# Performance work log

Hardware: AMD Instinct MI355X
Metric: run time of the kernel (lower is better)

## Reference

```python
import jax, jax.numpy as jnp
import numpy as np
import math

EPS = 1e-5

def _ln(x, g, b):
    mu = jnp.mean(x, axis=-1, keepdims=True)
    var = jnp.mean((x - mu) ** 2, axis=-1, keepdims=True)
    return (x - mu) * jax.lax.rsqrt(var + EPS) * g + b

def _phasor(x, phases, wv, bv, lno_g, lno_b, wo, bo):
    # x: [B,L,D]; phases buffer: [max_seq_len,D]
    B, L, D = x.shape
    ph = phases[:L][None]            # [1,L,D]
    c, s = jnp.cos(ph), jnp.sin(ph)
    v = x @ wv + bv                  # [B,L,D]
    mem_r = jnp.cumsum(v * c, axis=1)
    mem_i = jnp.cumsum(v * s, axis=1)
    retrieved = (mem_r * c + mem_i * s) / math.sqrt(D)
    return x + _ln(retrieved, lno_g, lno_b) @ wo + bo

def setup_inputs() -> dict:
    key = jax.random.key(0)
    ks = jax.random.split(key, 10)
    V, D, S, B, L = 32000, 1024, 2048, 4, 2048
    sc = 1.0 / math.sqrt(D)
    return {
        "tokens": jax.random.randint(ks[0], (B, L), 0, V, dtype=jnp.int32),
        "embed": jax.random.normal(ks[1], (V, D), jnp.float32) * sc,
        "ln1_g": jnp.ones((D,), jnp.float32), "ln1_b": jnp.zeros((D,), jnp.float32),
        "ph1": jax.random.normal(ks[2], (S, D), jnp.float32) * math.pi,
        "wv1": jax.random.normal(ks[3], (D, D), jnp.float32) * sc,
        "bv1": jnp.zeros((D,), jnp.float32),
        "lno1_g": jnp.ones((D,), jnp.float32), "lno1_b": jnp.zeros((D,), jnp.float32),
        "wo1": jax.random.normal(ks[4], (D, D), jnp.float32) * sc,
        "bo1": jnp.zeros((D,), jnp.float32),
        "ln2_g": jnp.ones((D,), jnp.float32), "ln2_b": jnp.zeros((D,), jnp.float32),
        "ph2": jax.random.normal(ks[5], (S, D), jnp.float32) * math.pi,
        "wv2": jax.random.normal(ks[6], (D, D), jnp.float32) * sc,
        "bv2": jnp.zeros((D,), jnp.float32),
        "lno2_g": jnp.ones((D,), jnp.float32), "lno2_b": jnp.zeros((D,), jnp.float32),
        "wo2": jax.random.normal(ks[7], (D, D), jnp.float32) * sc,
        "bo2": jnp.zeros((D,), jnp.float32),
        "ln3_g": jnp.ones((D,), jnp.float32), "ln3_b": jnp.zeros((D,), jnp.float32),
        "w_head": jax.random.normal(ks[8], (D, V), jnp.float32) * sc,
        "b_head": jnp.zeros((V,), jnp.float32),
    }

def reference(tokens, embed, ln1_g, ln1_b, ph1, wv1, bv1, lno1_g, lno1_b, wo1, bo1,
              ln2_g, ln2_b, ph2, wv2, bv2, lno2_g, lno2_b, wo2, bo2,
              ln3_g, ln3_b, w_head, b_head):
    h = embed[tokens]                                  # [B,L,D]
    h = h + _phasor(_ln(h, ln1_g, ln1_b), ph1, wv1, bv1, lno1_g, lno1_b, wo1, bo1)
    h = h + _phasor(_ln(h, ln2_g, ln2_b), ph2, wv2, bv2, lno2_g, lno2_b, wo2, bo2)
    return _ln(h, ln3_g, ln3_b) @ w_head + b_head      # [B,L,V]
```

## Files before the change

### kernel.cpp

```cpp
#include <hip/hip_runtime.h>
#include <hip/hip_bf16.h>
#include <math.h>

typedef __hip_bfloat16 bf16;
typedef __attribute__((ext_vector_type(8))) short bf16x8;
typedef __attribute__((ext_vector_type(4))) float f32x4;

#define GPTR(p) ((__attribute__((address_space(1))) void*)(void*)(p))
#define LPTR(p) ((__attribute__((address_space(3))) void*)(void*)(p))

static constexpr int kB = 4, kL = 2048, kD = 1024, kV = 32000;
static constexpr int kM = kB * kL;
static constexpr int kNC = 16, kCH = kL / kNC;

__global__ void k_sincos(const float* __restrict__ ph, float* __restrict__ c,
                         float* __restrict__ s, int n) {
  int i = blockIdx.x * 256 + threadIdx.x;
  if (i < n) {
    float sv, cv;
    sincosf(ph[i], &sv, &cv);
    c[i] = cv;
    s[i] = sv;
  }
}

__global__ void k_tcvt64(const float* __restrict__ in, bf16* __restrict__ out,
                         int R, int C) {
  __shared__ bf16 tile[64][66];
  int c0 = blockIdx.x * 64, r0 = blockIdx.y * 64;
  int tid = threadIdx.x;
  int cq = tid & 15;
  int rr = tid >> 4;
#pragma unroll
  for (int i = 0; i < 4; i++) {
    int r = rr + i * 16;
    float4 v = *(const float4*)(in + (size_t)(r0 + r) * C + c0 + cq * 4);
    tile[r][cq * 4 + 0] = __float2bfloat16(v.x);
    tile[r][cq * 4 + 1] = __float2bfloat16(v.y);
    tile[r][cq * 4 + 2] = __float2bfloat16(v.z);
    tile[r][cq * 4 + 3] = __float2bfloat16(v.w);
  }
  __syncthreads();
  int rb = tid & 7;
  int cc = tid >> 3;
#pragma unroll
  for (int i = 0; i < 2; i++) {
    int c = cc + i * 32;
    bf16x8 p;
#pragma unroll
    for (int j = 0; j < 8; j++) p[j] = *(const short*)&tile[rb * 8 + j][c];
    *(bf16x8*)(out + (size_t)(c0 + c) * R + r0 + rb * 8) = p;
  }
}

__global__ void k_embln(const int* __restrict__ tok, const float* __restrict__ emb,
                        const float* __restrict__ g, const float* __restrict__ b,
                        float* __restrict__ h, bf16* __restrict__ ob,
                        float* __restrict__ of) {
  int row = blockIdx.x;
  int tid = threadIdx.x;
  int t = tok[row];
  float4 v = ((const float4*)(emb + (size_t)t * kD))[tid];
  ((float4*)(h + (size_t)row * kD))[tid] = v;
  float sum = v.x + v.y + v.z + v.w;
  float sq = fmaf(v.x, v.x, fmaf(v.y, v.y, fmaf(v.z, v.z, v.w * v.w)));
#pragma unroll
  for (int o = 32; o > 0; o >>= 1) {
    sum += __shfl_down(sum, o);
    sq += __shfl_down(sq, o);
  }
  __shared__ float ss[4], sk[4];
  int w = tid >> 6;
  if ((tid & 63) == 0) { ss[w] = sum; sk[w] = sq; }
  __syncthreads();
  float ts = ss[0] + ss[1] + ss[2] + ss[3];
  float tq = sk[0] + sk[1] + sk[2] + sk[3];
  float mu = ts * (1.0f / kD);
  float var = tq * (1.0f / kD) - mu * mu;
  float rstd = rsqrtf(var + 1e-5f);
  float4 gg = ((const float4*)g)[tid];
  float4 bb = ((const float4*)b)[tid];
  float4 o;
  o.x = fmaf((v.x - mu) * rstd, gg.x, bb.x);
  o.y = fmaf((v.y - mu) * rstd, gg.y, bb.y);
  o.z = fmaf((v.z - mu) * rstd, gg.z, bb.z);
  o.w = fmaf((v.w - mu) * rstd, gg.w, bb.w);
  union { ushort4 u; bf16 hh[4]; } pk;
  pk.hh[0] = __float2bfloat16(o.x);
  pk.hh[1] = __float2bfloat16(o.y);
  pk.hh[2] = __float2bfloat16(o.z);
  pk.hh[3] = __float2bfloat16(o.w);
  *(ushort4*)(ob + (size_t)row * kD + tid * 4) = pk.u;
  ((float4*)(of + (size_t)row * kD))[tid] = o;
}

template <bool WF32>
__global__ void k_ln(const float* __restrict__ in, const float* __restrict__ g,
                     const float* __restrict__ b, bf16* __restrict__ ob,
                     float* __restrict__ of) {
  int row = blockIdx.x;
  int tid = threadIdx.x;
  const float4* x4 = (const float4*)(in + (size_t)row * kD);
  float4 v = x4[tid];
  float sum = v.x + v.y + v.z + v.w;
  float sq = fmaf(v.x, v.x, fmaf(v.y, v.y, fmaf(v.z, v.z, v.w * v.w)));
#pragma unroll
  for (int o = 32; o > 0; o >>= 1) {
    sum += __shfl_down(sum, o);
    sq += __shfl_down(sq, o);
  }
  __shared__ float ss[4], sk[4];
  int w = tid >> 6;
  if ((tid & 63) == 0) { ss[w] = sum; sk[w] = sq; }
  __syncthreads();
  float ts = ss[0] + ss[1] + ss[2] + ss[3];
  float tq = sk[0] + sk[1] + sk[2] + sk[3];
  float mu = ts * (1.0f / kD);
  float var = tq * (1.0f / kD) - mu * mu;
  float rstd = rsqrtf(var + 1e-5f);
  float4 gg = ((const float4*)g)[tid];
  float4 bb = ((const float4*)b)[tid];
  float4 o;
  o.x = fmaf((v.x - mu) * rstd, gg.x, bb.x);
  o.y = fmaf((v.y - mu) * rstd, gg.y, bb.y);
  o.z = fmaf((v.z - mu) * rstd, gg.z, bb.z);
  o.w = fmaf((v.w - mu) * rstd, gg.w, bb.w);
  union { ushort4 u; bf16 h[4]; } pk;
  pk.h[0] = __float2bfloat16(o.x);
  pk.h[1] = __float2bfloat16(o.y);
  pk.h[2] = __float2bfloat16(o.z);
  pk.h[3] = __float2bfloat16(o.w);
  *(ushort4*)(ob + (size_t)row * kD + tid * 4) = pk.u;
  if constexpr (WF32) {
    ((float4*)(of + (size_t)row * kD))[tid] = o;
  }
}

__global__ void k_scan_part(const float* __restrict__ v, const float* __restrict__ c,
                            const float* __restrict__ s, float* __restrict__ pr,
                            float* __restrict__ pi) {
  int tid = blockIdx.x * 256 + threadIdx.x;
  int d = tid & (kD - 1);
  int ch = (tid >> 10) & (kNC - 1);
  int b = tid >> 14;
  const float* vp = v + ((size_t)b * kL + ch * kCH) * kD + d;
  const float* cp = c + (size_t)(ch * kCH) * kD + d;
  const float* sp = s + (size_t)(ch * kCH) * kD + d;
  float ar = 0.f, ai = 0.f;
  for (int i = 0; i < kCH; i++) {
    float vv = vp[i * kD];
    ar = fmaf(vv, cp[i * kD], ar);
    ai = fmaf(vv, sp[i * kD], ai);
  }
  pr[tid] = ar;
  pi[tid] = ai;
}

__global__ void k_scan_apply(float* __restrict__ v, const float* __restrict__ c,
                             const float* __restrict__ s, const float* __restrict__ pr,
                             const float* __restrict__ pi) {
  int tid = blockIdx.x * 256 + threadIdx.x;
  int d = tid & (kD - 1);
  int ch = (tid >> 10) & (kNC - 1);
  int b = tid >> 14;
  float ar = 0.f, ai = 0.f;
  int pbase = (b << 14) + d;
  for (int cc = 0; cc < ch; cc++) {
    ar += pr[pbase + cc * kD];
    ai += pi[pbase + cc * kD];
  }
  float* vp = v + ((size_t)b * kL + ch * kCH) * kD + d;
  const float* cp = c + (size_t)(ch * kCH) * kD + d;
  const float* sp = s + (size_t)(ch * kCH) * kD + d;
  for (int i = 0; i < kCH; i++) {
    float vv = vp[i * kD];
    float cv = cp[i * kD], sv = sp[i * kD];
    ar = fmaf(vv, cv, ar);
    ai = fmaf(vv, sv, ai);
    vp[i * kD] = (ar * cv + ai * sv) * 0.03125f;
  }
}

template <int MODE>
__global__ __launch_bounds__(256) void k_gemm_bt(
    const bf16* __restrict__ A, const bf16* __restrict__ BT,
    const float* __restrict__ bias, const float* __restrict__ xres,
    const float* __restrict__ hres, float* __restrict__ Cout,
    int Md, int Nd, int Kd) {
  __shared__ __align__(16) bf16 As[128 * 32];
  __shared__ __align__(16) bf16 Bs[128 * 32];
  int nwg = gridDim.x * gridDim.y;
  int wg = blockIdx.y * gridDim.x + blockIdx.x;
  int per = nwg >> 3;
  int sw = (wg & 7) * per + (wg >> 3);
  int bm = sw % gridDim.x;
  int bn = sw / gridDim.x;
  int m0 = bm * 128, n0 = bn * 128;
  int tid = threadIdx.x;
  int wid = tid >> 6, lane = tid & 63;
  int wr = wid >> 1, wc = wid & 1;

  f32x4 acc[4][4];
#pragma unroll
  for (int i = 0; i < 4; i++)
#pragma unroll
    for (int j = 0; j < 4; j++) acc[i][j] = (f32x4){0.f, 0.f, 0.f, 0.f};

  const bf16* Abase = A + (size_t)m0 * Kd;
  const bf16* Bbase = BT + (size_t)n0 * Kd;
  int lr = lane >> 2;
  int lk = (lane & 3) * 8;
  int frow = lane & 15;
  int fk = (lane >> 4) * 8;

  for (int k0 = 0; k0 < Kd; k0 += 32) {
#pragma unroll
    for (int c = 0; c < 2; c++) {
      int ch = wid + c * 4;
      __builtin_amdgcn_global_load_lds(GPTR(Abase + (size_t)(ch * 16 + lr) * Kd + k0 + lk),
                                       LPTR(As + ch * 512), 16, 0, 0);
      __builtin_amdgcn_global_load_lds(GPTR(Bbase + (size_t)(ch * 16 + lr) * Kd + k0 + lk),
                                       LPTR(Bs + ch * 512), 16, 0, 0);
    }
    asm volatile("s_waitcnt vmcnt(0)" ::: "memory");
    __syncthreads();
    bf16x8 af[4], bfr[4];
#pragma unroll
    for (int i = 0; i < 4; i++) {
      af[i] = *(const bf16x8*)(As + (wr * 64 + i * 16 + frow) * 32 + fk);
      bfr[i] = *(const bf16x8*)(Bs + (wc * 64 + i * 16 + frow) * 32 + fk);
    }
#pragma unroll
    for (int i = 0; i < 4; i++)
#pragma unroll
      for (int j = 0; j < 4; j++)
        acc[i][j] = __builtin_amdgcn_mfma_f32_16x16x32_bf16(af[i], bfr[j], acc[i][j], 0, 0, 0);
    __syncthreads();
  }

  int cr = (lane >> 4) * 4;
  int ccl = lane & 15;
#pragma unroll
  for (int i = 0; i < 4; i++) {
#pragma unroll
    for (int j = 0; j < 4; j++) {
      int col = n0 + wc * 64 + j * 16 + ccl;
      float bv = bias[col];
#pragma unroll
      for (int r = 0; r < 4; r++) {
        int row = m0 + wr * 64 + i * 16 + cr + r;
        size_t idx = (size_t)row * Nd + col;
        float val = acc[i][j][r] + bv;
        if (MODE == 1) val += hres[idx] + xres[idx];
        Cout[idx] = val;
      }
    }
  }
}

__global__ __launch_bounds__(512, 2) void k_gemm256p8(
    const bf16* __restrict__ A, const bf16* __restrict__ BT,
    const float* __restrict__ bias, float* __restrict__ Cout,
    int Md, int Nd, int Kd) {
  __shared__ __align__(16) bf16 As[2][16384];
  __shared__ __align__(16) bf16 Bs[2][16384];

  int gx = gridDim.x;
  int wg = blockIdx.y * gx + blockIdx.x;
  int mch = gx >> 3;
  int xcd = wg & 7;
  int r = wg >> 3;
  int bm = xcd * mch + (r % mch);
  int bn = r / mch;
  int m0 = bm * 256, n0 = bn * 256;

  int tid = threadIdx.x;
  int wid = tid >> 6, lane = tid & 63;
  int wr = wid >> 2, wc = wid & 3;

  size_t KdS = (size_t)Kd;
  int srow = tid >> 3;
  int sk = (((tid & 7) ^ (srow & 7)) << 3);
  const bf16* aSrc = A + (size_t)(m0 + srow) * KdS + sk;
  const bf16* bSrc = BT + (size_t)(n0 + srow) * KdS + sk;
  int ldst = wid * 512;

#define STAGE_A(buf, h, t)                                                              \
  do {                                                                                  \
    __builtin_amdgcn_global_load_lds(GPTR(aSrc + (size_t)((h) * 128) * KdS + (t) * 64), \
                                     LPTR(&As[buf][(h) * 8192 + ldst]), 16, 0, 0);      \
    __builtin_amdgcn_global_load_lds(                                                   \
        GPTR(aSrc + (size_t)((h) * 128 + 64) * KdS + (t) * 64),                         \
        LPTR(&As[buf][(h) * 8192 + 4096 + ldst]), 16, 0, 0);                            \
  } while (0)
#define STAGE_B(buf, h, t)                                                              \
  do {                                                                                  \
    __builtin_amdgcn_global_load_lds(GPTR(bSrc + (size_t)((h) * 128) * KdS + (t) * 64), \
                                     LPTR(&Bs[buf][(h) * 8192 + ldst]), 16, 0, 0);      \
    __builtin_amdgcn_global_load_lds(                                                   \
        GPTR(bSrc + (size_t)((h) * 128 + 64) * KdS + (t) * 64),                         \
        LPTR(&Bs[buf][(h) * 8192 + 4096 + ldst]), 16, 0, 0);                            \
  } while (0)

  int frow = lane & 15;
  int khi = lane >> 4;
  int rx = frow & 7;
  int lk0 = ((khi) ^ rx) << 3;
  int lk1 = ((4 + khi) ^ rx) << 3;
  int wr16 = wr * 16;
  int wc64 = wc * 64;

  f32x4 acc[8][4];
#pragma unroll
  for (int m = 0; m < 8; m++)
#pragma unroll
    for (int n = 0; n < 4; n++) acc[m][n] = (f32x4){0.f, 0.f, 0.f, 0.f};

  const int NT = Kd >> 6;

  STAGE_A(0, 0, 0);
  STAGE_B(0, 0, 0);
  STAGE_B(0, 1, 0);
  STAGE_A(0, 1, 0);
  STAGE_A(1, 0, 1);
  STAGE_B(1, 0, 1);
  STAGE_B(1, 1, 1);
  asm volatile("s_waitcnt vmcnt(6)" ::: "memory");
  __builtin_amdgcn_s_barrier();
  __builtin_amdgcn_sched_barrier(0);

  for (int t = 0; t < NT; ++t) {
    int c = t & 1, o = c ^ 1;
    const bf16* Ac = As[c];
    const bf16* Bc = Bs[c];
    bf16x8 a[4][2], b[2][2], b2[2][2];

#pragma unroll
    for (int m = 0; m < 4; m++) {
      int ro = (m * 32 + wr16 + frow) * 64;
      a[m][0] = *(const bf16x8*)(Ac + ro + lk0);
      a[m][1] = *(const bf16x8*)(Ac + ro + lk1);
    }
#pragma unroll
    for (int n = 0; n < 2; n++) {
      int ro = (wc64 + n * 16 + frow) * 64;
      b[n][0] = *(const bf16x8*)(Bc + ro + lk0);
      b[n][1] = *(const bf16x8*)(Bc + ro + lk1);
    }
    if (t + 1 < NT) STAGE_A(o, 1, t + 1);
    __builtin_amdgcn_s_barrier();
    asm volatile("s_waitcnt lgkmcnt(0)" ::: "memory");
    __builtin_amdgcn_sched_barrier(0);
    __builtin_amdgcn_s_setprio(1);
#pragma unroll
    for (int m = 0; m < 4; m++)
#pragma unroll
      for (int n = 0; n < 2; n++) {
        acc[m][n] = __builtin_amdgcn_mfma_f32_16x16x32_bf16(a[m][0], b[n][0], acc[m][n], 0, 0, 0);
        acc[m][n] = __builtin_amdgcn_mfma_f32_16x16x32_bf16(a[m][1], b[n][1], acc[m][n], 0, 0, 0);
      }
    __builtin_amdgcn_s_setprio(0);
    __builtin_amdgcn_s_barrier();
    __builtin_amdgcn_sched_barrier(0);

#pragma unroll
    for (int n = 0; n < 2; n++) {
      int ro = (wc64 + (n + 2) * 16 + frow) * 64;
      b2[n][0] = *(const bf16x8*)(Bc + ro + lk0);
      b2[n][1] = *(const bf16x8*)(Bc + ro + lk1);
    }
    if (t + 2 < NT) STAGE_A(c, 0, t + 2);
    __builtin_amdgcn_s_barrier();
    asm volatile("s_waitcnt lgkmcnt(0)" ::: "memory");
    __builtin_amdgcn_sched_barrier(0);
    __builtin_amdgcn_s_setprio(1);
#pragma unroll
    for (int m = 0; m < 4; m++)
#pragma unroll
      for (int n = 0; n < 2; n++) {
        acc[m][n + 2] = __builtin_amdgcn_mfma_f32_16x16x32_bf16(a[m][0], b2[n][0], acc[m][n + 2], 0, 0, 0);
        acc[m][n + 2] = __builtin_amdgcn_mfma_f32_16x16x32_bf16(a[m][1], b2[n][1], acc[m][n + 2], 0, 0, 0);
      }
    __builtin_amdgcn_s_setprio(0);
    __builtin_amdgcn_s_barrier();
    __builtin_amdgcn_sched_barrier(0);

#pragma unroll
    for (int m = 0; m < 4; m++) {
      int ro = ((m + 4) * 32 + wr16 + frow) * 64;
      a[m][0] = *(const bf16x8*)(Ac + ro + lk0);
      a[m][1] = *(const bf16x8*)(Ac + ro + lk1);
    }
    if (t + 2 < NT) STAGE_B(c, 0, t + 2);
    __builtin_amdgcn_s_barrier();
    asm volatile("s_waitcnt lgkmcnt(0)" ::: "memory");
    __builtin_amdgcn_sched_barrier(0);
    __builtin_amdgcn_s_setprio(1);
#pragma unroll
    for (int m = 0; m < 4; m++)
#pragma unroll
      for (int n = 0; n < 2; n++) {
        acc[m + 4][n] = __builtin_amdgcn_mfma_f32_16x16x32_bf16(a[m][0], b[n][0], acc[m + 4][n], 0, 0, 0);
        acc[m + 4][n] = __builtin_amdgcn_mfma_f32_16x16x32_bf16(a[m][1], b[n][1], acc[m + 4][n], 0, 0, 0);
      }
    __builtin_amdgcn_s_setprio(0);
    __builtin_amdgcn_s_barrier();
    __builtin_amdgcn_sched_barrier(0);

    if (t + 2 < NT) STAGE_B(c, 1, t + 2);
    __builtin_amdgcn_s_barrier();
    __builtin_amdgcn_sched_barrier(0);
    __builtin_amdgcn_s_setprio(1);
#pragma unroll
    for (int m = 0; m < 4; m++)
#pragma unroll
      for (int n = 0; n < 2; n++) {
        acc[m + 4][n + 2] = __builtin_amdgcn_mfma_f32_16x16x32_bf16(a[m][0], b2[n][0], acc[m + 4][n + 2], 0, 0, 0);
        acc[m + 4][n + 2] = __builtin_amdgcn_mfma_f32_16x16x32_bf16(a[m][1], b2[n][1], acc[m + 4][n + 2], 0, 0, 0);
      }
    __builtin_amdgcn_s_setprio(0);
    if (t < NT - 2) {
      asm volatile("s_waitcnt vmcnt(6)" ::: "memory");
    } else if (t == NT - 2) {
      asm volatile("s_waitcnt vmcnt(0)" ::: "memory");
    }
    __builtin_amdgcn_s_barrier();
    __builtin_amdgcn_sched_barrier(0);
  }
#undef STAGE_A
#undef STAGE_B

  float* eplds = (float*)&As[0][0] + wid * 1088;
  int q = lane & 15;
  int g = lane >> 4;
  float bv[4];
#pragma unroll
  for (int n = 0; n < 4; n++) bv[n] = bias[n0 + wc64 + n * 16 + q];
#pragma unroll
  for (int m = 0; m < 8; m++) {
#pragma unroll
    for (int n = 0; n < 4; n++)
#pragma unroll
      for (int r2 = 0; r2 < 4; r2++)
        eplds[(g * 4 + r2) * 68 + n * 16 + q] = acc[m][n][r2] + bv[n];
    asm volatile("s_waitcnt lgkmcnt(0)" ::: "memory");
    __builtin_amdgcn_sched_barrier(0);
#pragma unroll
    for (int rr = 0; rr < 4; rr++) {
      f32x4 v4 = *(const f32x4*)(eplds + (rr * 4 + g) * 68 + q * 4);
      int row = m0 + m * 32 + wr16 + rr * 4 + g;
      __builtin_nontemporal_store(
          v4, (f32x4*)(Cout + (size_t)row * Nd + n0 + wc64 + q * 4));
    }
    asm volatile("s_waitcnt lgkmcnt(0)" ::: "memory");
    __builtin_amdgcn_sched_barrier(0);
  }
}

extern "C" void kernel_launch(void* const* d_in, const int* in_sizes, int n_in,
                              void* d_out, int out_size, void* d_ws, size_t ws_size,
                              hipStream_t stream) {
  const int* tokens   = (const int*)d_in[0];
  const float* embed  = (const float*)d_in[1];
  const float* ln1_g  = (const float*)d_in[2];
  const float* ln1_b  = (const float*)d_in[3];
  const float* ph1    = (const float*)d_in[4];
  const float* wv1    = (const float*)d_in[5];
  const float* bv1    = (const float*)d_in[6];
  const float* lno1_g = (const float*)d_in[7];
  const float* lno1_b = (const float*)d_in[8];
  const float* wo1    = (const float*)d_in[9];
  const float* bo1    = (const float*)d_in[10];
  const float* ln2_g  = (const float*)d_in[11];
  const float* ln2_b  = (const float*)d_in[12];
  const float* ph2    = (const float*)d_in[13];
  const float* wv2    = (const float*)d_in[14];
  const float* bv2    = (const float*)d_in[15];
  const float* lno2_g = (const float*)d_in[16];
  const float* lno2_b = (const float*)d_in[17];
  const float* wo2    = (const float*)d_in[18];
  const float* bo2    = (const float*)d_in[19];
  const float* ln3_g  = (const float*)d_in[20];
  const float* ln3_b  = (const float*)d_in[21];
  const float* w_head = (const float*)d_in[22];
  const float* b_head = (const float*)d_in[23];

  float* out = (float*)d_out;

  char* ws = (char*)d_ws;
  bf16* whT  = (bf16*)ws;
  bf16* wv1T = whT + (size_t)kV * kD;
  bf16* wo1T = wv1T + (size_t)kD * kD;
  bf16* wv2T = wo1T + (size_t)kD * kD;
  bf16* wo2T = wv2T + (size_t)kD * kD;
  bf16* xb   = wo2T + (size_t)kD * kD;

  float* h  = out;
  float* xf = h + (size_t)kM * kD;
  float* vb = xf + (size_t)kM * kD;
  float* ct = vb + (size_t)kM * kD;
  float* st = ct + (size_t)kL * kD;
  float* pr = st + (size_t)kL * kD;
  float* pi = pr + (size_t)kB * kNC * kD;

  k_tcvt64<<<dim3(kD / 64, kD / 64), 256, 0, stream>>>(wv1, wv1T, kD, kD);
  k_tcvt64<<<dim3(kD / 64, kD / 64), 256, 0, stream>>>(wo1, wo1T, kD, kD);
  k_tcvt64<<<dim3(kD / 64, kD / 64), 256, 0, stream>>>(wv2, wv2T, kD, kD);
  k_tcvt64<<<dim3(kD / 64, kD / 64), 256, 0, stream>>>(wo2, wo2T, kD, kD);
  k_tcvt64<<<dim3(kV / 64, kD / 64), 256, 0, stream>>>(w_head, whT, kD, kV);

  const int scanBlocks = kB * kNC * kD / 256;

  k_sincos<<<(kL * kD + 255) / 256, 256, 0, stream>>>(ph1, ct, st, kL * kD);
  k_embln<<<kM, 256, 0, stream>>>(tokens, embed, ln1_g, ln1_b, h, xb, xf);
  k_gemm_bt<0><<<dim3(kM / 128, kD / 128), 256, 0, stream>>>(xb, wv1T, bv1, nullptr, nullptr,
                                                             vb, kM, kD, kD);
  k_scan_part<<<scanBlocks, 256, 0, stream>>>(vb, ct, st, pr, pi);
  k_scan_apply<<<scanBlocks, 256, 0, stream>>>(vb, ct, st, pr, pi);
  k_ln<false><<<kM, 256, 0, stream>>>(vb, lno1_g, lno1_b, xb, nullptr);
  k_gemm_bt<1><<<dim3(kM / 128, kD / 128), 256, 0, stream>>>(xb, wo1T, bo1, xf, h,
                                                             h, kM, kD, kD);

  k_sincos<<<(kL * kD + 255) / 256, 256, 0, stream>>>(ph2, ct, st, kL * kD);
  k_ln<true><<<kM, 256, 0, stream>>>(h, ln2_g, ln2_b, xb, xf);
  k_gemm_bt<0><<<dim3(kM / 128, kD / 128), 256, 0, stream>>>(xb, wv2T, bv2, nullptr, nullptr,
                                                             vb, kM, kD, kD);
  k_scan_part<<<scanBlocks, 256, 0, stream>>>(vb, ct, st, pr, pi);
  k_scan_apply<<<scanBlocks, 256, 0, stream>>>(vb, ct, st, pr, pi);
  k_ln<false><<<kM, 256, 0, stream>>>(vb, lno2_g, lno2_b, xb, nullptr);
  k_gemm_bt<1><<<dim3(kM / 128, kD / 128), 256, 0, stream>>>(xb, wo2T, bo2, xf, h,
                                                             h, kM, kD, kD);

  k_ln<false><<<kM, 256, 0, stream>>>(h, ln3_g, ln3_b, xb, nullptr);
  k_gemm256p8<<<dim3(kM / 256, kV / 256), 512, 0, stream>>>(xb, whT, b_head, out,
                                                            kM, kV, kD);
}
```

Baseline: 962.3 us.

## Replace DxD GEMM with double-buffered 128x256 swizzled-LDS pipelined kernel

Replaces the simple single-buffered 128x128 BK=32 GEMM used for the four DxD projections with a 512-thread 128x256 tile kernel. It uses BK=64, double-buffered LDS with XOR-swizzled layout, and staggered async global-to-LDS prefetch of the next tiles during MFMA phases. It also adds explicit barriers, priority hints and XCD-aware block mapping. The aim is to hide memory latency, avoid LDS bank conflicts and raise MFMA utilisation, at the cost of more LDS per block and only 256 blocks per GEMM.

```diff
diff --git a/kernel.cpp b/kernel.cpp
--- a/kernel.cpp
+++ b/kernel.cpp
@@ -182,23 +182,57 @@
 }
 
 template <int MODE>
-__global__ __launch_bounds__(256) void k_gemm_bt(
+__global__ __launch_bounds__(512, 2) void k_gemm_bt2(
     const bf16* __restrict__ A, const bf16* __restrict__ BT,
     const float* __restrict__ bias, const float* __restrict__ xres,
     const float* __restrict__ hres, float* __restrict__ Cout,
     int Md, int Nd, int Kd) {
-  __shared__ __align__(16) bf16 As[128 * 32];
-  __shared__ __align__(16) bf16 Bs[128 * 32];
-  int nwg = gridDim.x * gridDim.y;
-  int wg = blockIdx.y * gridDim.x + blockIdx.x;
-  int per = nwg >> 3;
-  int sw = (wg & 7) * per + (wg >> 3);
-  int bm = sw % gridDim.x;
-  int bn = sw / gridDim.x;
-  int m0 = bm * 128, n0 = bn * 128;
+  __shared__ __align__(16) bf16 As[2][8192];
+  __shared__ __align__(16) bf16 Bs[2][16384];
+
+  int gx = gridDim.x;
+  int wg = blockIdx.y * gx + blockIdx.x;
+  int mch = gx >> 3;
+  int xcd = wg & 7;
+  int r = wg >> 3;
+  int bm = xcd * mch + (r % mch);
+  int bn = r / mch;
+  int m0 = bm * 128, n0 = bn * 256;
+
   int tid = threadIdx.x;
   int wid = tid >> 6, lane = tid & 63;
-  int wr = wid >> 1, wc = wid & 1;
+  int wr = wid >> 2, wc = wid & 3;
+
+  size_t KdS = (size_t)Kd;
+  int srow = tid >> 3;
+  int sk = (((tid & 7) ^ (srow & 7)) << 3);
+  const bf16* aSrc = A + (size_t)(m0 + srow) * KdS + sk;
+  const bf16* bSrc = BT + (size_t)(n0 + srow) * KdS + sk;
+  int ldst = wid * 512;
+
+#define STAGE_A2(buf, t)                                                                \
+  do {                                                                                  \
+    __builtin_amdgcn_global_load_lds(GPTR(aSrc + (size_t)(t) * 64),                     \
+                                     LPTR(&As[buf][ldst]), 16, 0, 0);                   \
+    __builtin_amdgcn_global_load_lds(GPTR(aSrc + (size_t)64 * KdS + (size_t)(t) * 64),  \
+                                     LPTR(&As[buf][4096 + ldst]), 16, 0, 0);            \
+  } while (0)
+#define STAGE_B2(buf, h, t)                                                             \
+  do {                                                                                  \
+    __builtin_amdgcn_global_load_lds(GPTR(bSrc + (size_t)((h) * 128) * KdS + (t) * 64), \
+                                     LPTR(&Bs[buf][(h) * 8192 + ldst]), 16, 0, 0);      \
+    __builtin_amdgcn_global_load_lds(                                                   \
+        GPTR(bSrc + (size_t)((h) * 128 + 64) * KdS + (t) * 64),                         \
+        LPTR(&Bs[buf][(h) * 8192 + 4096 + ldst]), 16, 0, 0);                            \
+  } while (0)
+
+  int frow = lane & 15;
+  int khi = lane >> 4;
+  int rx = frow & 7;
+  int lk0 = ((khi) ^ rx) << 3;
+  int lk1 = ((4 + khi) ^ rx) << 3;
+  int wr16 = wr * 16;
+  int wc64 = wc * 64;
 
   f32x4 acc[4][4];
 #pragma unroll
@@ -206,51 +240,96 @@
 #pragma unroll
     for (int j = 0; j < 4; j++) acc[i][j] = (f32x4){0.f, 0.f, 0.f, 0.f};
 
-  const bf16* Abase = A + (size_t)m0 * Kd;
-  const bf16* Bbase = BT + (size_t)n0 * Kd;
-  int lr = lane >> 2;
-  int lk = (lane & 3) * 8;
-  int frow = lane & 15;
-  int fk = (lane >> 4) * 8;
-
-  for (int k0 = 0; k0 < Kd; k0 += 32) {
-#pragma unroll
-    for (int c = 0; c < 2; c++) {
-      int ch = wid + c * 4;
-      __builtin_amdgcn_global_load_lds(GPTR(Abase + (size_t)(ch * 16 + lr) * Kd + k0 + lk),
-                                       LPTR(As + ch * 512), 16, 0, 0);
-      __builtin_amdgcn_global_load_lds(GPTR(Bbase + (size_t)(ch * 16 + lr) * Kd + k0 + lk),
-                                       LPTR(Bs + ch * 512), 16, 0, 0);
-    }
-    asm volatile("s_waitcnt vmcnt(0)" ::: "memory");
-    __syncthreads();
-    bf16x8 af[4], bfr[4];
-#pragma unroll
-    for (int i = 0; i < 4; i++) {
-      af[i] = *(const bf16x8*)(As + (wr * 64 + i * 16 + frow) * 32 + fk);
-      bfr[i] = *(const bf16x8*)(Bs + (wc * 64 + i * 16 + frow) * 32 + fk);
-    }
-#pragma unroll
-    for (int i = 0; i < 4; i++)
-#pragma unroll
-      for (int j = 0; j < 4; j++)
-        acc[i][j] = __builtin_amdgcn_mfma_f32_16x16x32_bf16(af[i], bfr[j], acc[i][j], 0, 0, 0);
-    __syncthreads();
-  }
+  const int NT = Kd >> 6;
+
+  STAGE_A2(0, 0);
+  STAGE_B2(0, 0, 0);
+  STAGE_B2(0, 1, 0);
+  STAGE_A2(1, 1);
+  asm volatile("s_waitcnt vmcnt(2)" ::: "memory");
+  __builtin_amdgcn_s_barrier();
+  __builtin_amdgcn_sched_barrier(0);
+
+  for (int t = 0; t < NT; ++t) {
+    int c = t & 1, o = c ^ 1;
+    const bf16* Ac = As[c];
+    const bf16* Bc = Bs[c];
+    bf16x8 a[4][2], b[2][2], b2[2][2];
+
+#pragma unroll
+    for (int m = 0; m < 4; m++) {
+      int ro = (m * 32 + wr16 + frow) * 64;
+      a[m][0] = *(const bf16x8*)(Ac + ro + lk0);
+      a[m][1] = *(const bf16x8*)(Ac + ro + lk1);
+    }
+#pragma unroll
+    for (int n = 0; n < 2; n++) {
+      int ro = (wc64 + n * 16 + frow) * 64;
+      b[n][0] = *(const bf16x8*)(Bc + ro + lk0);
+      b[n][1] = *(const bf16x8*)(Bc + ro + lk1);
+    }
+    if (t + 1 < NT) {
+      STAGE_B2(o, 0, t + 1);
+      STAGE_B2(o, 1, t + 1);
+    }
+    __builtin_amdgcn_s_barrier();
+    asm volatile("s_waitcnt lgkmcnt(0)" ::: "memory");
+    __builtin_amdgcn_sched_barrier(0);
+    __builtin_amdgcn_s_setprio(1);
+#pragma unroll
+    for (int m = 0; m < 4; m++)
+#pragma unroll
+      for (int n = 0; n < 2; n++) {
+        acc[m][n] = __builtin_amdgcn_mfma_f32_16x16x32_bf16(a[m][0], b[n][0], acc[m][n], 0, 0, 0);
+        acc[m][n] = __builtin_amdgcn_mfma_f32_16x16x32_bf16(a[m][1], b[n][1], acc[m][n], 0, 0, 0);
+      }
+    __builtin_amdgcn_s_setprio(0);
+    __builtin_amdgcn_s_barrier();
+    __builtin_amdgcn_sched_barrier(0);
+
+#pragma unroll
+    for (int n = 0; n < 2; n++) {
+      int ro = (wc64 + (n + 2) * 16 + frow) * 64;
+      b2[n][0] = *(const bf16x8*)(Bc + ro + lk0);
+      b2[n][1] = *(const bf16x8*)(Bc + ro + lk1);
+    }
+    if (t + 2 < NT) STAGE_A2(c, t + 2);
+    __builtin_amdgcn_s_barrier();
+    asm volatile("s_waitcnt lgkmcnt(0)" ::: "memory");
+    __builtin_amdgcn_sched_barrier(0);
+    __builtin_amdgcn_s_setprio(1);
+#pragma unroll
+    for (int m = 0; m < 4; m++)
+#pragma unroll
+      for (int n = 0; n < 2; n++) {
+        acc[m][n + 2] = __builtin_amdgcn_mfma_f32_16x16x32_bf16(a[m][0], b2[n][0], acc[m][n + 2], 0, 0, 0);
+        acc[m][n + 2] = __builtin_amdgcn_mfma_f32_16x16x32_bf16(a[m][1], b2[n][1], acc[m][n + 2], 0, 0, 0);
+      }
+    __builtin_amdgcn_s_setprio(0);
+    if (t < NT - 2) {
+      asm volatile("s_waitcnt vmcnt(2)" ::: "memory");
+    } else if (t == NT - 2) {
+      asm volatile("s_waitcnt vmcnt(0)" ::: "memory");
+    }
+    __builtin_amdgcn_s_barrier();
+    __builtin_amdgcn_sched_barrier(0);
+  }
+#undef STAGE_A2
+#undef STAGE_B2
 
   int cr = (lane >> 4) * 4;
   int ccl = lane & 15;
 #pragma unroll
-  for (int i = 0; i < 4; i++) {
-#pragma unroll
-    for (int j = 0; j < 4; j++) {
-      int col = n0 + wc * 64 + j * 16 + ccl;
+  for (int m = 0; m < 4; m++) {
+#pragma unroll
+    for (int n = 0; n < 4; n++) {
+      int col = n0 + wc64 + n * 16 + ccl;
       float bv = bias[col];
 #pragma unroll
-      for (int r = 0; r < 4; r++) {
-        int row = m0 + wr * 64 + i * 16 + cr + r;
+      for (int r2 = 0; r2 < 4; r2++) {
+        int row = m0 + m * 32 + wr16 + cr + r2;
         size_t idx = (size_t)row * Nd + col;
-        float val = acc[i][j][r] + bv;
+        float val = acc[m][n][r2] + bv;
         if (MODE == 1) val += hres[idx] + xres[idx];
         Cout[idx] = val;
       }
@@ -513,23 +592,23 @@
 
   k_sincos<<<(kL * kD + 255) / 256, 256, 0, stream>>>(ph1, ct, st, kL * kD);
   k_embln<<<kM, 256, 0, stream>>>(tokens, embed, ln1_g, ln1_b, h, xb, xf);
-  k_gemm_bt<0><<<dim3(kM / 128, kD / 128), 256, 0, stream>>>(xb, wv1T, bv1, nullptr, nullptr,
-                                                             vb, kM, kD, kD);
+  k_gemm_bt2<0><<<dim3(kM / 128, kD / 256), 512, 0, stream>>>(xb, wv1T, bv1, nullptr, nullptr,
+                                                              vb, kM, kD, kD);
   k_scan_part<<<scanBlocks, 256, 0, stream>>>(vb, ct, st, pr, pi);
   k_scan_apply<<<scanBlocks, 256, 0, stream>>>(vb, ct, st, pr, pi);
   k_ln<false><<<kM, 256, 0, stream>>>(vb, lno1_g, lno1_b, xb, nullptr);
-  k_gemm_bt<1><<<dim3(kM / 128, kD / 128), 256, 0, stream>>>(xb, wo1T, bo1, xf, h,
-                                                             h, kM, kD, kD);
+  k_gemm_bt2<1><<<dim3(kM / 128, kD / 256), 512, 0, stream>>>(xb, wo1T, bo1, xf, h,
+                                                              h, kM, kD, kD);
 
   k_sincos<<<(kL * kD + 255) / 256, 256, 0, stream>>>(ph2, ct, st, kL * kD);
   k_ln<true><<<kM, 256, 0, stream>>>(h, ln2_g, ln2_b, xb, xf);
-  k_gemm_bt<0><<<dim3(kM / 128, kD / 128), 256, 0, stream>>>(xb, wv2T, bv2, nullptr, nullptr,
-                                                             vb, kM, kD, kD);
+  k_gemm_bt2<0><<<dim3(kM / 128, kD / 256), 512, 0, stream>>>(xb, wv2T, bv2, nullptr, nullptr,
+                                                              vb, kM, kD, kD);
   k_scan_part<<<scanBlocks, 256, 0, stream>>>(vb, ct, st, pr, pi);
   k_scan_apply<<<scanBlocks, 256, 0, stream>>>(vb, ct, st, pr, pi);
   k_ln<false><<<kM, 256, 0, stream>>>(vb, lno2_g, lno2_b, xb, nullptr);
-  k_gemm_bt<1><<<dim3(kM / 128, kD / 128), 256, 0, stream>>>(xb, wo2T, bo2, xf, h,
-                                                             h, kM, kD, kD);
+  k_gemm_bt2<1><<<dim3(kM / 128, kD / 256), 512, 0, stream>>>(xb, wo2T, bo2, xf, h,
+                                                              h, kM, kD, kD);
 
   k_ln<false><<<kM, 256, 0, stream>>>(h, ln3_g, ln3_b, xb, nullptr);
   k_gemm256p8<<<dim3(kM / 256, kV / 256), 512, 0, stream>>>(xb, whT, b_head, out,
```

Result: faster. 930.3 us (-3.3%).
